# Optimization experiments

Hardware: AMD Instinct MI355X
Metric: run time of the kernel (lower is better)

## Reference

```python
import jax, jax.numpy as jnp
import numpy as np

B, L, D, H = 4, 2048, 1024, 16
DK = D // H


def setup_inputs() -> dict:
    key = jax.random.key(0)
    ks = jax.random.split(key, 8)
    def n(k, shape, s=1.0):
        return jax.random.normal(k, shape, dtype=jnp.float32) * s
    return {
        "q": n(ks[0], (B, L, D)),
        "k": n(ks[1], (B, L, D)),
        "v": n(ks[2], (B, L, D)),
        "Wq": n(ks[3], (D, D), 0.02), "bq": jnp.zeros((D,), jnp.float32),
        "Wk": n(ks[4], (D, D), 0.02), "bk": jnp.zeros((D,), jnp.float32),
        "Wv": n(ks[5], (D, D), 0.02), "bv": jnp.zeros((D,), jnp.float32),
        "Wo": n(ks[6], (D, D), 0.02), "bo": jnp.zeros((D,), jnp.float32),
        # relative-position table, torch: nn.Parameter(zeros(2L-1, d_k)); random here
        "w_rel": n(ks[7], (2 * L - 1, DK), 0.02),
    }


def reference(q, k, v, Wq, bq, Wk, bk, Wv, bv, Wo, bo, w_rel):
    # Dropout is identity in eval mode (reference baseline).
    bs, Lq, _ = q.shape
    qh = (q @ Wq.T + bq).reshape(bs, Lq, H, DK).transpose(0, 2, 1, 3)  # (B,H,L,dk)
    kh = (k @ Wk.T + bk).reshape(bs, -1, H, DK).transpose(0, 2, 1, 3)
    vh = (v @ Wv.T + bv).reshape(bs, -1, H, DK).transpose(0, 2, 1, 3)

    # content-content scores
    scores = jnp.einsum('bhid,bhjd->bhij', qh, kh)  # (B,H,L,L)

    # relative bias. torch unfold: rel_pos[i, d, j] = w_rel[i + j, d]
    # bias[b,h,i,j] = sum_d qh[b,h,i,d] * w_rel[i+j, d]
    # Compute t = q . w_rel over the 2L-1 axis, then skew-gather (avoids LxLxdk tensor).
    t = jnp.einsum('bhid,rd->bhir', qh, w_rel)  # (B,H,L,2L-1)
    idx = jnp.arange(Lq)[:, None] + jnp.arange(Lq)[None, :]  # (L,L) values i+j
    bias = jnp.take_along_axis(t, idx[None, None], axis=-1)  # (B,H,L,L)

    attn = jax.nn.softmax((scores + bias) / jnp.sqrt(jnp.float32(DK)), axis=-1)
    out = jnp.einsum('bhij,bhjd->bhid', attn, vh)  # (B,H,L,dk)
    concat = out.transpose(0, 2, 1, 3).reshape(bs, Lq, D)
    return concat @ Wo.T + bo
```

## Files before the change

### kernel.cpp

```cpp
#include <hip/hip_runtime.h>

typedef __attribute__((ext_vector_type(8))) short bf16x8;
typedef __attribute__((ext_vector_type(4))) float f32x4;
typedef unsigned short u16;
typedef unsigned int u32;

constexpr int kB = 4, kL = 2048, kD = 1024, kH = 16, kDK = 64;
constexpr int kR = kB * kL;
constexpr long kWrelMax = 2 * kL - 2;
constexpr float kQScale = 0.125f * 1.44269504088896f;

__device__ inline float fexp2(float x) { return __builtin_amdgcn_exp2f(x); }

__device__ inline u16 f2bf(float x) {
    union { float f; u32 u; } v; v.f = x;
    u32 r = v.u + 0x7FFFu + ((v.u >> 16) & 1u);
    return (u16)(r >> 16);
}
__device__ inline void splitf(float x, u16& hi, u16& lo) {
    union { float f; u32 u; } v; v.f = x;
    u32 hu = v.u & 0xFFFF0000u;
    hi = (u16)(hu >> 16);
    union { u32 u; float f; } hf; hf.u = hu;
    union { float f; u32 u; } l; l.f = x - hf.f;
    lo = (u16)(l.u >> 16);
}
__device__ inline f32x4 MFMA(bf16x8 a, bf16x8 b, f32x4 c) {
    return __builtin_amdgcn_mfma_f32_16x16x32_bf16(a, b, c, 0, 0, 0);
}
__device__ __forceinline__ void gll16(const u16* g, u16* l) {
    __builtin_amdgcn_global_load_lds(
        (const __attribute__((address_space(1))) u32*)g,
        (__attribute__((address_space(3))) u32*)l, 16, 0, 0);
}

__global__ void split4x4_kernel(const float* __restrict__ i0, const float* __restrict__ i1,
                                const float* __restrict__ i2, const float* __restrict__ i3,
                                u16* __restrict__ h0, u16* __restrict__ h1,
                                u16* __restrict__ h2, u16* __restrict__ h3,
                                u16* __restrict__ l0, u16* __restrict__ l1,
                                u16* __restrict__ l2, u16* __restrict__ l3, int n4) {
    int idx = blockIdx.x * blockDim.x + threadIdx.x;
    if (idx >= n4) return;
    const float* in = blockIdx.y == 0 ? i0 : blockIdx.y == 1 ? i1 : blockIdx.y == 2 ? i2 : i3;
    u16* hi = blockIdx.y == 0 ? h0 : blockIdx.y == 1 ? h1 : blockIdx.y == 2 ? h2 : h3;
    u16* lo = blockIdx.y == 0 ? l0 : blockIdx.y == 1 ? l1 : blockIdx.y == 2 ? l2 : l3;
    float4 x = reinterpret_cast<const float4*>(in)[idx];
    ushort4 h, l;
    splitf(x.x, h.x, l.x); splitf(x.y, h.y, l.y);
    splitf(x.z, h.z, l.z); splitf(x.w, h.w, l.w);
    reinterpret_cast<ushort4*>(hi)[idx] = h;
    reinterpret_cast<ushort4*>(lo)[idx] = l;
}
__global__ void split4_kernel(const float* __restrict__ in,
                              u16* __restrict__ hi, u16* __restrict__ lo, int n4) {
    int idx = blockIdx.x * blockDim.x + threadIdx.x;
    if (idx >= n4) return;
    float4 x = reinterpret_cast<const float4*>(in)[idx];
    ushort4 h, l;
    splitf(x.x, h.x, l.x); splitf(x.y, h.y, l.y);
    splitf(x.z, h.z, l.z); splitf(x.w, h.w, l.w);
    reinterpret_cast<ushort4*>(hi)[idx] = h;
    reinterpret_cast<ushort4*>(lo)[idx] = l;
}

__global__ __launch_bounds__(256) void proj3(
    const float* __restrict__ Aq, const float* __restrict__ Ak, const float* __restrict__ Av,
    const u16* __restrict__ Bqh, const u16* __restrict__ Bkh, const u16* __restrict__ Bvh,
    const float* __restrict__ bq, const float* __restrict__ bk, const float* __restrict__ bv,
    u16* __restrict__ Yq, u16* __restrict__ Yk, u16* __restrict__ Yv)
{
    __shared__ __align__(16) u16 Ash[128 * 32], Asl[128 * 32];
    __shared__ __align__(16) u16 Bsh[128 * 32];

    const int z = blockIdx.z;
    const float* Af32 = z == 0 ? Aq : z == 1 ? Ak : Av;
    const u16* Bgh    = z == 0 ? Bqh : z == 1 ? Bkh : Bvh;
    const float* bias = z == 0 ? bq : z == 1 ? bk : bv;
    u16* Yh           = z == 0 ? Yq : z == 1 ? Yk : Yv;
    const float scale = z == 0 ? kQScale : 1.0f;

    const int tid = threadIdx.x;
    const int row0 = blockIdx.x * 128, col0 = blockIdx.y * 128;
    const int w = tid >> 6, lane = tid & 63;
    const int s = lane & 15, g = lane >> 4;
    const int wrow = w >> 1, wcol = w & 1;
    const int srow = tid >> 1;
    const int skq  = (tid & 1) * 16;

    const f32x4 fz = {0.f, 0.f, 0.f, 0.f};
    f32x4 acc[4][4];
    #pragma unroll
    for (int m = 0; m < 4; ++m)
        #pragma unroll
        for (int n = 0; n < 4; ++n) acc[m][n] = fz;

    float4 aR[4];
    bf16x8 bRh[2];

    auto loadA = [&](int k0) {
        const float* p = &Af32[(size_t)(row0 + srow) * kD + k0 + skq];
        aR[0] = *(const float4*)(p);
        aR[1] = *(const float4*)(p + 4);
        aR[2] = *(const float4*)(p + 8);
        aR[3] = *(const float4*)(p + 12);
    };
    auto loadB = [&](int k0) {
        const u16* ph = &Bgh[(size_t)(col0 + srow) * kD + k0 + skq];
        bRh[0] = *(const bf16x8*)ph; bRh[1] = *(const bf16x8*)(ph + 8);
    };
    auto writeAB = [&]() {
        const int c0 = skq >> 3, sw = srow & 3;
        bf16x8 h0, h1, l0, l1;
        const float* af = (const float*)aR;
        #pragma unroll
        for (int q = 0; q < 8; ++q) {
            u16 hh, ll;
            splitf(af[q], hh, ll);     h0[q] = (short)hh; l0[q] = (short)ll;
            splitf(af[8 + q], hh, ll); h1[q] = (short)hh; l1[q] = (short)ll;
        }
        *(bf16x8*)&Ash[srow * 32 + (((c0    ) ^ sw) << 3)] = h0;
        *(bf16x8*)&Ash[srow * 32 + (((c0 + 1) ^ sw) << 3)] = h1;
        *(bf16x8*)&Asl[srow * 32 + (((c0    ) ^ sw) << 3)] = l0;
        *(bf16x8*)&Asl[srow * 32 + (((c0 + 1) ^ sw) << 3)] = l1;
        *(bf16x8*)&Bsh[srow * 32 + (((c0    ) ^ sw) << 3)] = bRh[0];
        *(bf16x8*)&Bsh[srow * 32 + (((c0 + 1) ^ sw) << 3)] = bRh[1];
    };

    loadA(0); loadB(0);
    for (int k0 = 0; k0 < kD; k0 += 32) {
        __syncthreads();
        writeAB();
        __syncthreads();
        if (k0 + 32 < kD) { loadA(k0 + 32); loadB(k0 + 32); }

        bf16x8 fAh[4], fAl[4], fBh[4];
        #pragma unroll
        for (int m = 0; m < 4; ++m) {
            int ar = wrow * 64 + m * 16 + s;
            int off = ar * 32 + ((g ^ (ar & 3)) << 3);
            fAh[m] = *(const bf16x8*)&Ash[off];
            fAl[m] = *(const bf16x8*)&Asl[off];
        }
        #pragma unroll
        for (int n = 0; n < 4; ++n) {
            int bc = wcol * 64 + n * 16 + s;
            int off = bc * 32 + ((g ^ (bc & 3)) << 3);
            fBh[n] = *(const bf16x8*)&Bsh[off];
        }
        #pragma unroll
        for (int m = 0; m < 4; ++m)
            #pragma unroll
            for (int n = 0; n < 4; ++n) {
                acc[m][n] = MFMA(fAh[m], fBh[n], acc[m][n]);
                acc[m][n] = MFMA(fAl[m], fBh[n], acc[m][n]);
            }
    }

    #pragma unroll
    for (int n = 0; n < 4; ++n) {
        const int colg = col0 + wcol * 64 + n * 16 + s;
        const float bv = bias[colg];
        #pragma unroll
        for (int m = 0; m < 4; ++m) {
            const int rowg = row0 + wrow * 64 + m * 16 + (g << 2);
            if (z == 2) {
                const int b = rowg >> 11, i = rowg & (kL - 1);
                const int h = colg >> 6, d = colg & 63;
                ushort4 o4;
                o4.x = f2bf(acc[m][n][0] + bv);
                o4.y = f2bf(acc[m][n][1] + bv);
                o4.z = f2bf(acc[m][n][2] + bv);
                o4.w = f2bf(acc[m][n][3] + bv);
                *(ushort4*)&Yh[(((size_t)b * kH + h) * kDK + d) * kL + i] = o4;
            } else {
                #pragma unroll
                for (int r = 0; r < 4; ++r) {
                    float val = (acc[m][n][r] + bv) * scale;
                    const int rg = rowg + r;
                    const int b = rg >> 11, i = rg & (kL - 1);
                    const int h = colg >> 6, d = colg & 63;
                    Yh[(((size_t)b * kH + h) * kL + i) * kDK + d] = f2bf(val);
                }
            }
        }
    }
}

__global__ __launch_bounds__(256) void out_gemm(
    const u16* __restrict__ Agh, const u16* __restrict__ Agl,
    const u16* __restrict__ Bgh, const u16* __restrict__ Bgl,
    const float* __restrict__ bias, float* __restrict__ Yf)
{
    __shared__ __align__(16) u16 Ash[128 * 32], Asl[128 * 32];
    __shared__ __align__(16) u16 Bsh[128 * 32], Bsl[128 * 32];

    const int tid = threadIdx.x;
    const int row0 = blockIdx.x * 128, col0 = blockIdx.y * 128;
    const int w = tid >> 6, lane = tid & 63;
    const int s = lane & 15, g = lane >> 4;
    const int wrow = w >> 1, wcol = w & 1;
    const int srow = tid >> 1;
    const int skq  = (tid & 1) * 16;

    const f32x4 fz = {0.f, 0.f, 0.f, 0.f};
    f32x4 acc[4][4];
    #pragma unroll
    for (int m = 0; m < 4; ++m)
        #pragma unroll
        for (int n = 0; n < 4; ++n) acc[m][n] = fz;

    bf16x8 aRh[2], aRl[2], bRh[2], bRl[2];
    auto loadA = [&](int k0) {
        const u16* ph = &Agh[(size_t)(row0 + srow) * kD + k0 + skq];
        const u16* pl = &Agl[(size_t)(row0 + srow) * kD + k0 + skq];
        aRh[0] = *(const bf16x8*)ph; aRh[1] = *(const bf16x8*)(ph + 8);
        aRl[0] = *(const bf16x8*)pl; aRl[1] = *(const bf16x8*)(pl + 8);
    };
    auto loadB = [&](int k0) {
        const u16* ph = &Bgh[(size_t)(col0 + srow) * kD + k0 + skq];
        const u16* pl = &Bgl[(size_t)(col0 + srow) * kD + k0 + skq];
        bRh[0] = *(const bf16x8*)ph; bRh[1] = *(const bf16x8*)(ph + 8);
        bRl[0] = *(const bf16x8*)pl; bRl[1] = *(const bf16x8*)(pl + 8);
    };
    auto writeAB = [&]() {
        const int c0 = skq >> 3, sw = srow & 3;
        *(bf16x8*)&Ash[srow * 32 + (((c0    ) ^ sw) << 3)] = aRh[0];
        *(bf16x8*)&Ash[srow * 32 + (((c0 + 1) ^ sw) << 3)] = aRh[1];
        *(bf16x8*)&Asl[srow * 32 + (((c0    ) ^ sw) << 3)] = aRl[0];
        *(bf16x8*)&Asl[srow * 32 + (((c0 + 1) ^ sw) << 3)] = aRl[1];
        *(bf16x8*)&Bsh[srow * 32 + (((c0    ) ^ sw) << 3)] = bRh[0];
        *(bf16x8*)&Bsh[srow * 32 + (((c0 + 1) ^ sw) << 3)] = bRh[1];
        *(bf16x8*)&Bsl[srow * 32 + (((c0    ) ^ sw) << 3)] = bRl[0];
        *(bf16x8*)&Bsl[srow * 32 + (((c0 + 1) ^ sw) << 3)] = bRl[1];
    };

    loadA(0); loadB(0);
    for (int k0 = 0; k0 < kD; k0 += 32) {
        __syncthreads();
        writeAB();
        __syncthreads();
        if (k0 + 32 < kD) { loadA(k0 + 32); loadB(k0 + 32); }

        bf16x8 fAh[4], fAl[4], fBh[4], fBl[4];
        #pragma unroll
        for (int m = 0; m < 4; ++m) {
            int ar = wrow * 64 + m * 16 + s;
            int off = ar * 32 + ((g ^ (ar & 3)) << 3);
            fAh[m] = *(const bf16x8*)&Ash[off];
            fAl[m] = *(const bf16x8*)&Asl[off];
        }
        #pragma unroll
        for (int n = 0; n < 4; ++n) {
            int bc = wcol * 64 + n * 16 + s;
            int off = bc * 32 + ((g ^ (bc & 3)) << 3);
            fBh[n] = *(const bf16x8*)&Bsh[off];
            fBl[n] = *(const bf16x8*)&Bsl[off];
        }
        #pragma unroll
        for (int m = 0; m < 4; ++m)
            #pragma unroll
            for (int n = 0; n < 4; ++n) {
                acc[m][n] = MFMA(fAh[m], fBh[n], acc[m][n]);
                acc[m][n] = MFMA(fAl[m], fBh[n], acc[m][n]);
                acc[m][n] = MFMA(fAh[m], fBl[n], acc[m][n]);
            }
    }

    #pragma unroll
    for (int n = 0; n < 4; ++n) {
        const int colg = col0 + wcol * 64 + n * 16 + s;
        const float bv = bias[colg];
        #pragma unroll
        for (int m = 0; m < 4; ++m) {
            const int rowg = row0 + wrow * 64 + m * 16 + (g << 2);
            #pragma unroll
            for (int r = 0; r < 4; ++r)
                Yf[(size_t)(rowg + r) * kD + colg] = acc[m][n][r] + bv;
        }
    }
}

__global__ __launch_bounds__(256, 2) void attn3(
    const u16* __restrict__ Qh,
    const u16* __restrict__ Kg, const u16* __restrict__ VT,
    const u16* __restrict__ Wr,
    u16* __restrict__ Ch, u16* __restrict__ Cl)
{
    __shared__ __align__(16) u16 Ksh[2][64 * 64];
    __shared__ __align__(16) u16 Vsh[2][64 * 64];
    __shared__ __align__(16) u16 Wsh[2][64 * 64];
    __shared__ __align__(16) u16 Ps[4][16 * 64];
    __shared__ __align__(16) u16 Tb[64 * 132];

    const int tid = threadIdx.x;
    const int w = tid >> 6, lane = tid & 63;
    const int s = lane & 15, g = lane >> 4;
    const int bh = blockIdx.y, i0 = blockIdx.x * 64;
    const int b = bh >> 4, h = bh & 15;

    const int srow = tid >> 3;
    const int sc = tid & 7;

    auto stageK = [&](int buf, int t) {
        const u16* base = Kg + ((size_t)bh * kL + (size_t)t * 64) * kDK;
        #pragma unroll
        for (int it = 0; it < 2; ++it) {
            int r = srow + it * 32;
            gll16(base + r * 64 + ((sc ^ (r & 7)) << 3), &Ksh[buf][it * 2048 + w * 512]);
        }
    };
    auto stageV = [&](int buf, int t) {
        #pragma unroll
        for (int it = 0; it < 2; ++it) {
            int d = srow + it * 32;
            const u16* src = VT + ((size_t)bh * kDK + d) * kL + t * 64 + ((sc ^ (d & 7)) << 3);
            gll16(src, &Vsh[buf][it * 2048 + w * 512]);
        }
    };
    auto stageW = [&](int buf, int c) {
        #pragma unroll
        for (int it = 0; it < 2; ++it) {
            int r = srow + it * 32;
            long row = (long)i0 + 64L * c + r;
            if (row > kWrelMax) row = kWrelMax;
            gll16(Wr + row * 64 + ((sc ^ (r & 7)) << 3), &Wsh[buf][it * 2048 + w * 512]);
        }
    };

    int foff[4][2];
    #pragma unroll
    for (int n = 0; n < 4; ++n)
        #pragma unroll
        for (int ks = 0; ks < 2; ++ks) {
            int row = n * 16 + s;
            foff[n][ks] = row * 64 + (((ks * 4 + g) ^ (row & 7)) << 3);
        }
    int prd[2];
    #pragma unroll
    for (int ks = 0; ks < 2; ++ks)
        prd[ks] = s * 64 + (((ks * 4 + g) ^ (s & 7)) << 3);
    int pwr[4];
    #pragma unroll
    for (int jn = 0; jn < 4; ++jn) {
        int c = 2 * jn + (g >> 1);
        pwr[jn] = s * 64 + ((c ^ (s & 7)) << 3) + (g & 1) * 4;
    }

    const size_t qbase = ((size_t)bh * kL + i0 + w * 16 + s) * kDK + g * 8;
    bf16x8 qh[2];
    qh[0] = *(const bf16x8*)&Qh[qbase];
    qh[1] = *(const bf16x8*)&Qh[qbase + 32];

    const f32x4 fz = {0.f, 0.f, 0.f, 0.f};
    const int ilS = w * 16 + s;
    const int ilw = w * 16 + g * 4;

    auto computeT = [&](int c, int buf) {
        f32x4 tacc[4];
        #pragma unroll
        for (int un = 0; un < 4; ++un) {
            bf16x8 wf0 = *(const bf16x8*)&Wsh[buf][foff[un][0]];
            bf16x8 wf1 = *(const bf16x8*)&Wsh[buf][foff[un][1]];
            tacc[un] = MFMA(qh[0], wf0, fz);
            tacc[un] = MFMA(qh[1], wf1, tacc[un]);
        }
        const int cb = c * 64 - w * 16 + s - g * 4;
        #pragma unroll
        for (int un = 0; un < 4; ++un)
            #pragma unroll
            for (int r = 0; r < 4; ++r) {
                int key = (cb + un * 16 - r) & 127;
                Tb[(ilw + r) * 132 + key] =
                    (u16)(__float_as_uint(tacc[un][r]) >> 16);
            }
    };

    f32x4 sacc[4];
    auto loadBias = [&](int t) {
        #pragma unroll
        for (int jn = 0; jn < 4; ++jn) {
            int kb = (t * 64 + jn * 16 + g * 4) & 127;
            uint2 tw = *(const uint2*)&Tb[ilS * 132 + kb];
            sacc[jn][0] = __uint_as_float(tw.x << 16);
            sacc[jn][1] = __uint_as_float(tw.x & 0xFFFF0000u);
            sacc[jn][2] = __uint_as_float(tw.y << 16);
            sacc[jn][3] = __uint_as_float(tw.y & 0xFFFF0000u);
        }
    };

    bf16x8 ones;
    #pragma unroll
    for (int q = 0; q < 8; ++q) ones[q] = (short)0x3F80;

    stageK(0, 0); stageV(0, 0); stageW(0, 0); stageW(1, 1);
    __syncthreads();
    computeT(0, 0); computeT(1, 1);
    loadBias(0);
    __syncthreads();
    stageW(0, 2);
    __syncthreads();

    f32x4 oacc[4] = {fz, fz, fz, fz};
    f32x4 lacc = fz;

    for (int t = 0; t < 32; ++t) {
        const int cur = t & 1, nxt = cur ^ 1;
        if (t < 31) { stageK(nxt, t + 1); stageV(nxt, t + 1); }
        if (t < 30) stageW(nxt, t + 3);
        if (t < 31) computeT(t + 2, cur);

        __builtin_amdgcn_s_setprio(1);
        #pragma unroll
        for (int jn = 0; jn < 4; ++jn)
            #pragma unroll
            for (int ks = 0; ks < 2; ++ks) {
                bf16x8 kf = *(const bf16x8*)&Ksh[cur][foff[jn][ks]];
                sacc[jn] = MFMA(kf, qh[ks], sacc[jn]);
            }
        __builtin_amdgcn_s_setprio(0);

        #pragma unroll
        for (int jn = 0; jn < 4; ++jn) {
            u32 a0 = __float_as_uint(fexp2(sacc[jn][0])) & 0xFFFF0000u;
            u32 a1 = __float_as_uint(fexp2(sacc[jn][1])) & 0xFFFF0000u;
            u32 a2 = __float_as_uint(fexp2(sacc[jn][2])) & 0xFFFF0000u;
            u32 a3 = __float_as_uint(fexp2(sacc[jn][3])) & 0xFFFF0000u;
            uint2 pw;
            pw.x = a1 | (a0 >> 16);
            pw.y = a3 | (a2 >> 16);
            *(uint2*)&Ps[w][pwr[jn]] = pw;
        }

        if (t < 31) loadBias(t + 1);

        __builtin_amdgcn_s_setprio(1);
        #pragma unroll
        for (int ks = 0; ks < 2; ++ks) {
            bf16x8 pf = *(const bf16x8*)&Ps[w][prd[ks]];
            lacc = MFMA(pf, ones, lacc);
            #pragma unroll
            for (int dn = 0; dn < 4; ++dn) {
                bf16x8 vf = *(const bf16x8*)&Vsh[cur][foff[dn][ks]];
                oacc[dn] = MFMA(pf, vf, oacc[dn]);
            }
        }
        __builtin_amdgcn_s_setprio(0);
        __syncthreads();
    }

    float invr[4];
    #pragma unroll
    for (int r = 0; r < 4; ++r) invr[r] = 1.0f / lacc[r];

    #pragma unroll
    for (int dn = 0; dn < 4; ++dn)
        #pragma unroll
        for (int r = 0; r < 4; ++r) {
            const int ig = i0 + w * 16 + g * 4 + r;
            float val = oacc[dn][r] * invr[r];
            u16 hh, ll; splitf(val, hh, ll);
            size_t o = ((size_t)(b * kL + ig)) * kD + h * kDK + dn * 16 + s;
            Ch[o] = hh; Cl[o] = ll;
        }
}

extern "C" void kernel_launch(void* const* d_in, const int* in_sizes, int n_in,
                              void* d_out, int out_size, void* d_ws, size_t ws_size,
                              hipStream_t stream) {
    const float* q    = (const float*)d_in[0];
    const float* k    = (const float*)d_in[1];
    const float* v    = (const float*)d_in[2];
    const float* Wq   = (const float*)d_in[3];
    const float* bq   = (const float*)d_in[4];
    const float* Wk   = (const float*)d_in[5];
    const float* bk   = (const float*)d_in[6];
    const float* Wv   = (const float*)d_in[7];
    const float* bv   = (const float*)d_in[8];
    const float* Wo   = (const float*)d_in[9];
    const float* bo   = (const float*)d_in[10];
    const float* wrel = (const float*)d_in[11];
    float* out = (float*)d_out;

    u16* p = (u16*)d_ws;
    const size_t nW = (size_t)kD * kD;
    const size_t nR = (size_t)(2 * kL - 1) * kDK;
    const size_t nT = (size_t)kB * kL * kD;
    u16* wqh = p; p += nW;  u16* wql = p; p += nW;
    u16* wkh = p; p += nW;  u16* wkl = p; p += nW;
    u16* wvh = p; p += nW;  u16* wvl = p; p += nW;
    u16* woh = p; p += nW;  u16* wol = p; p += nW;
    u16* wrh = p; p += nR;  u16* wrl = p; p += nR;
    u16* qhh = p; p += nT;
    u16* khh = p; p += nT;
    u16* vT  = p; p += nT;
    u16* cch = p; p += nT;  u16* ccl = p; p += nT;

    hipLaunchKernelGGL(split4x4_kernel, dim3(1024, 4), dim3(256), 0, stream,
                       Wq, Wk, Wv, Wo, wqh, wkh, wvh, woh, wql, wkl, wvl, wol,
                       (int)(nW / 4));
    hipLaunchKernelGGL(split4_kernel, dim3(256), dim3(256), 0, stream,
                       wrel, wrh, wrl, (int)(nR / 4));

    dim3 blk(256);
    hipLaunchKernelGGL(proj3, dim3(kR / 128, kD / 128, 3), blk, 0, stream,
                       q, k, v, wqh, wkh, wvh, bq, bk, bv, qhh, khh, vT);

    hipLaunchKernelGGL(attn3, dim3(kL / 64, kB * kH), blk, 0, stream,
                       qhh, khh, vT, wrh, cch, ccl);

    hipLaunchKernelGGL(out_gemm, dim3(kR / 128, kD / 128), blk, 0, stream,
                       cch, ccl, woh, wol, bo, out);
}
```

Baseline: 391.1 us.

## Double-buffer projection GEMMs with direct global-to-LDS loads and remap attention blocks

Both projection GEMMs now keep two LDS buffers. The bf16 operands are loaded with direct global-to-LDS loads (gll16) into the next buffer while MFMAs run on the current one, which removes one barrier per k-step and the register staging. In proj3 the fp32 A operand is still split in registers, but its write and next load are moved after the compute. The attention kernel also remaps its block index so consecutive blocks are spread across heads, likely to balance XCD/L2 placement. The cost is double the LDS per GEMM block, which may lower occupancy.

```diff
diff --git a/kernel.cpp b/kernel.cpp
--- a/kernel.cpp
+++ b/kernel.cpp
@@ -70,8 +70,8 @@
     const float* __restrict__ bq, const float* __restrict__ bk, const float* __restrict__ bv,
     u16* __restrict__ Yq, u16* __restrict__ Yk, u16* __restrict__ Yv)
 {
-    __shared__ __align__(16) u16 Ash[128 * 32], Asl[128 * 32];
-    __shared__ __align__(16) u16 Bsh[128 * 32];
+    __shared__ __align__(16) u16 Ash[2][128 * 32], Asl[2][128 * 32];
+    __shared__ __align__(16) u16 Bsh[2][128 * 32];
 
     const int z = blockIdx.z;
     const float* Af32 = z == 0 ? Aq : z == 1 ? Ak : Av;
@@ -88,6 +88,19 @@
     const int srow = tid >> 1;
     const int skq  = (tid & 1) * 16;
 
+    const u16* bsrc[2];
+    #pragma unroll
+    for (int it = 0; it < 2; ++it) {
+        int row = w * 32 + it * 16 + (lane >> 2);
+        int cl = (lane & 3) ^ (row & 3);
+        bsrc[it] = &Bgh[(size_t)(col0 + row) * kD + cl * 8];
+    }
+    auto gllB = [&](int buf, int k0) {
+        #pragma unroll
+        for (int it = 0; it < 2; ++it)
+            gll16(bsrc[it] + k0, &Bsh[buf][(w * 128 + it * 64) * 8]);
+    };
+
     const f32x4 fz = {0.f, 0.f, 0.f, 0.f};
     f32x4 acc[4][4];
     #pragma unroll
@@ -96,8 +109,6 @@
         for (int n = 0; n < 4; ++n) acc[m][n] = fz;
 
     float4 aR[4];
-    bf16x8 bRh[2];
-
     auto loadA = [&](int k0) {
         const float* p = &Af32[(size_t)(row0 + srow) * kD + k0 + skq];
         aR[0] = *(const float4*)(p);
@@ -105,11 +116,7 @@
         aR[2] = *(const float4*)(p + 8);
         aR[3] = *(const float4*)(p + 12);
     };
-    auto loadB = [&](int k0) {
-        const u16* ph = &Bgh[(size_t)(col0 + srow) * kD + k0 + skq];
-        bRh[0] = *(const bf16x8*)ph; bRh[1] = *(const bf16x8*)(ph + 8);
-    };
-    auto writeAB = [&]() {
+    auto writeA = [&](int buf) {
         const int c0 = skq >> 3, sw = srow & 3;
         bf16x8 h0, h1, l0, l1;
         const float* af = (const float*)aR;
@@ -119,34 +126,35 @@
             splitf(af[q], hh, ll);     h0[q] = (short)hh; l0[q] = (short)ll;
             splitf(af[8 + q], hh, ll); h1[q] = (short)hh; l1[q] = (short)ll;
         }
-        *(bf16x8*)&Ash[srow * 32 + (((c0    ) ^ sw) << 3)] = h0;
-        *(bf16x8*)&Ash[srow * 32 + (((c0 + 1) ^ sw) << 3)] = h1;
-        *(bf16x8*)&Asl[srow * 32 + (((c0    ) ^ sw) << 3)] = l0;
-        *(bf16x8*)&Asl[srow * 32 + (((c0 + 1) ^ sw) << 3)] = l1;
-        *(bf16x8*)&Bsh[srow * 32 + (((c0    ) ^ sw) << 3)] = bRh[0];
-        *(bf16x8*)&Bsh[srow * 32 + (((c0 + 1) ^ sw) << 3)] = bRh[1];
-    };
-
-    loadA(0); loadB(0);
+        *(bf16x8*)&Ash[buf][srow * 32 + (((c0    ) ^ sw) << 3)] = h0;
+        *(bf16x8*)&Ash[buf][srow * 32 + (((c0 + 1) ^ sw) << 3)] = h1;
+        *(bf16x8*)&Asl[buf][srow * 32 + (((c0    ) ^ sw) << 3)] = l0;
+        *(bf16x8*)&Asl[buf][srow * 32 + (((c0 + 1) ^ sw) << 3)] = l1;
+    };
+
+    loadA(0);
+    gllB(0, 0);
+    writeA(0);
+    loadA(32);
+    __syncthreads();
+
     for (int k0 = 0; k0 < kD; k0 += 32) {
-        __syncthreads();
-        writeAB();
-        __syncthreads();
-        if (k0 + 32 < kD) { loadA(k0 + 32); loadB(k0 + 32); }
+        const int cur = (k0 >> 5) & 1, nxt = cur ^ 1;
+        if (k0 + 32 < kD) gllB(nxt, k0 + 32);
 
         bf16x8 fAh[4], fAl[4], fBh[4];
         #pragma unroll
         for (int m = 0; m < 4; ++m) {
             int ar = wrow * 64 + m * 16 + s;
             int off = ar * 32 + ((g ^ (ar & 3)) << 3);
-            fAh[m] = *(const bf16x8*)&Ash[off];
-            fAl[m] = *(const bf16x8*)&Asl[off];
+            fAh[m] = *(const bf16x8*)&Ash[cur][off];
+            fAl[m] = *(const bf16x8*)&Asl[cur][off];
         }
         #pragma unroll
         for (int n = 0; n < 4; ++n) {
             int bc = wcol * 64 + n * 16 + s;
             int off = bc * 32 + ((g ^ (bc & 3)) << 3);
-            fBh[n] = *(const bf16x8*)&Bsh[off];
+            fBh[n] = *(const bf16x8*)&Bsh[cur][off];
         }
         #pragma unroll
         for (int m = 0; m < 4; ++m)
@@ -155,6 +163,10 @@
                 acc[m][n] = MFMA(fAh[m], fBh[n], acc[m][n]);
                 acc[m][n] = MFMA(fAl[m], fBh[n], acc[m][n]);
             }
+
+        if (k0 + 32 < kD) writeA(nxt);
+        if (k0 + 64 < kD) loadA(k0 + 64);
+        __syncthreads();
     }
 
     #pragma unroll
@@ -192,16 +204,37 @@
     const u16* __restrict__ Bgh, const u16* __restrict__ Bgl,
     const float* __restrict__ bias, float* __restrict__ Yf)
 {
-    __shared__ __align__(16) u16 Ash[128 * 32], Asl[128 * 32];
-    __shared__ __align__(16) u16 Bsh[128 * 32], Bsl[128 * 32];
+    __shared__ __align__(16) u16 Ash[2][128 * 32], Asl[2][128 * 32];
+    __shared__ __align__(16) u16 Bsh[2][128 * 32], Bsl[2][128 * 32];
 
     const int tid = threadIdx.x;
     const int row0 = blockIdx.x * 128, col0 = blockIdx.y * 128;
     const int w = tid >> 6, lane = tid & 63;
     const int s = lane & 15, g = lane >> 4;
     const int wrow = w >> 1, wcol = w & 1;
-    const int srow = tid >> 1;
-    const int skq  = (tid & 1) * 16;
+
+    const u16* srcAh[2]; const u16* srcAl[2];
+    const u16* srcBh[2]; const u16* srcBl[2];
+    #pragma unroll
+    for (int it = 0; it < 2; ++it) {
+        int row = w * 32 + it * 16 + (lane >> 2);
+        int cl = (lane & 3) ^ (row & 3);
+        size_t oa = (size_t)(row0 + row) * kD + cl * 8;
+        size_t ob = (size_t)(col0 + row) * kD + cl * 8;
+        srcAh[it] = Agh + oa; srcAl[it] = Agl + oa;
+        srcBh[it] = Bgh + ob; srcBl[it] = Bgl + ob;
+    }
+    auto gll4 = [&](int buf, int k0) {
+        #pragma unroll
+        for (int it = 0; it < 2; ++it) {
+            u16* d = (u16*)((w * 128 + it * 64) * 8);
+            gll16(srcAh[it] + k0, &Ash[buf][(w * 128 + it * 64) * 8]);
+            gll16(srcAl[it] + k0, &Asl[buf][(w * 128 + it * 64) * 8]);
+            gll16(srcBh[it] + k0, &Bsh[buf][(w * 128 + it * 64) * 8]);
+            gll16(srcBl[it] + k0, &Bsl[buf][(w * 128 + it * 64) * 8]);
+            (void)d;
+        }
+    };
 
     const f32x4 fz = {0.f, 0.f, 0.f, 0.f};
     f32x4 acc[4][4];
@@ -210,52 +243,27 @@
         #pragma unroll
         for (int n = 0; n < 4; ++n) acc[m][n] = fz;
 
-    bf16x8 aRh[2], aRl[2], bRh[2], bRl[2];
-    auto loadA = [&](int k0) {
-        const u16* ph = &Agh[(size_t)(row0 + srow) * kD + k0 + skq];
-        const u16* pl = &Agl[(size_t)(row0 + srow) * kD + k0 + skq];
-        aRh[0] = *(const bf16x8*)ph; aRh[1] = *(const bf16x8*)(ph + 8);
-        aRl[0] = *(const bf16x8*)pl; aRl[1] = *(const bf16x8*)(pl + 8);
-    };
-    auto loadB = [&](int k0) {
-        const u16* ph = &Bgh[(size_t)(col0 + srow) * kD + k0 + skq];
-        const u16* pl = &Bgl[(size_t)(col0 + srow) * kD + k0 + skq];
-        bRh[0] = *(const bf16x8*)ph; bRh[1] = *(const bf16x8*)(ph + 8);
-        bRl[0] = *(const bf16x8*)pl; bRl[1] = *(const bf16x8*)(pl + 8);
-    };
-    auto writeAB = [&]() {
-        const int c0 = skq >> 3, sw = srow & 3;
-        *(bf16x8*)&Ash[srow * 32 + (((c0    ) ^ sw) << 3)] = aRh[0];
-        *(bf16x8*)&Ash[srow * 32 + (((c0 + 1) ^ sw) << 3)] = aRh[1];
-        *(bf16x8*)&Asl[srow * 32 + (((c0    ) ^ sw) << 3)] = aRl[0];
-        *(bf16x8*)&Asl[srow * 32 + (((c0 + 1) ^ sw) << 3)] = aRl[1];
-        *(bf16x8*)&Bsh[srow * 32 + (((c0    ) ^ sw) << 3)] = bRh[0];
-        *(bf16x8*)&Bsh[srow * 32 + (((c0 + 1) ^ sw) << 3)] = bRh[1];
-        *(bf16x8*)&Bsl[srow * 32 + (((c0    ) ^ sw) << 3)] = bRl[0];
-        *(bf16x8*)&Bsl[srow * 32 + (((c0 + 1) ^ sw) << 3)] = bRl[1];
-    };
-
-    loadA(0); loadB(0);
+    gll4(0, 0);
+    __syncthreads();
+
     for (int k0 = 0; k0 < kD; k0 += 32) {
-        __syncthreads();
-        writeAB();
-        __syncthreads();
-        if (k0 + 32 < kD) { loadA(k0 + 32); loadB(k0 + 32); }
+        const int cur = (k0 >> 5) & 1, nxt = cur ^ 1;
+        if (k0 + 32 < kD) gll4(nxt, k0 + 32);
 
         bf16x8 fAh[4], fAl[4], fBh[4], fBl[4];
         #pragma unroll
         for (int m = 0; m < 4; ++m) {
             int ar = wrow * 64 + m * 16 + s;
             int off = ar * 32 + ((g ^ (ar & 3)) << 3);
-            fAh[m] = *(const bf16x8*)&Ash[off];
-            fAl[m] = *(const bf16x8*)&Asl[off];
+            fAh[m] = *(const bf16x8*)&Ash[cur][off];
+            fAl[m] = *(const bf16x8*)&Asl[cur][off];
         }
         #pragma unroll
         for (int n = 0; n < 4; ++n) {
             int bc = wcol * 64 + n * 16 + s;
             int off = bc * 32 + ((g ^ (bc & 3)) << 3);
-            fBh[n] = *(const bf16x8*)&Bsh[off];
-            fBl[n] = *(const bf16x8*)&Bsl[off];
+            fBh[n] = *(const bf16x8*)&Bsh[cur][off];
+            fBl[n] = *(const bf16x8*)&Bsl[cur][off];
         }
         #pragma unroll
         for (int m = 0; m < 4; ++m)
@@ -265,6 +273,7 @@
                 acc[m][n] = MFMA(fAl[m], fBh[n], acc[m][n]);
                 acc[m][n] = MFMA(fAh[m], fBl[n], acc[m][n]);
             }
+        __syncthreads();
     }
 
     #pragma unroll
@@ -296,7 +305,9 @@
     const int tid = threadIdx.x;
     const int w = tid >> 6, lane = tid & 63;
     const int s = lane & 15, g = lane >> 4;
-    const int bh = blockIdx.y, i0 = blockIdx.x * 64;
+    const int pb = blockIdx.x + 32 * blockIdx.y;
+    const int lb = (pb & 7) * 256 + (pb >> 3);
+    const int bh = lb >> 5, i0 = (lb & 31) * 64;
     const int b = bh >> 4, h = bh & 15;
 
     const int srow = tid >> 3;
```

After: 420.2 us, median of 2. 7.5% more time.
